# Performance work log

Measured on AMD Instinct MI355X. Metric: run time of the kernel, lower is better.

## Reference

```python
import jax, jax.numpy as jnp
import numpy as np

STRIDE = 4
HEADS = 8
KSIZE = 5
PAD_L = 4  # causal: kernel_size - 1


def _layernorm(x, g, b, eps=1e-5):
    mu = jnp.mean(x, axis=-1, keepdims=True)
    var = jnp.mean((x - mu) ** 2, axis=-1, keepdims=True)
    return (x - mu) * jax.lax.rsqrt(var + eps) * g + b


def setup_inputs() -> dict:
    key = jax.random.key(0)
    ks = jax.random.split(key, 6)
    B, T, C = 8, 2048, 1024
    D = 4096
    x = jax.random.normal(ks[0], (B, T, C), dtype=jnp.float32)
    W_proj = jax.random.normal(ks[1], (C * STRIDE, D), dtype=jnp.float32) * 0.02
    b_proj = jnp.zeros((D,), dtype=jnp.float32)
    ln_g = jnp.ones((D,), dtype=jnp.float32)
    ln_b = jnp.zeros((D,), dtype=jnp.float32)
    W_wgen = jax.random.normal(ks[2], (D, HEADS * KSIZE), dtype=jnp.float32) * 0.02
    b_wgen = jnp.zeros((HEADS * KSIZE,), dtype=jnp.float32)
    W_ff = jax.random.normal(ks[3], (D, D), dtype=jnp.float32) * 0.02
    b_ff = jnp.zeros((D,), dtype=jnp.float32)
    return {"x": x, "W_proj": W_proj, "b_proj": b_proj, "ln_g": ln_g, "ln_b": ln_b,
            "W_wgen": W_wgen, "b_wgen": b_wgen, "W_ff": W_ff, "b_ff": b_ff}


def reference(x, W_proj, b_proj, ln_g, ln_b, W_wgen, b_wgen, W_ff, b_ff):
    B, T, C = x.shape
    folded_T = T // STRIDE
    # fold time into channels, then dense projection to llm_dim
    xf = x[:, : folded_T * STRIDE].reshape(B, folded_T, C * STRIDE)
    h = xf @ W_proj + b_proj  # [B, Tf, D]
    D = h.shape[-1]
    R = D // HEADS
    # LConv1DBlock with norm_before + dynamic conv + (linear, relu, dropout p=0) + residual
    res = h
    y = _layernorm(h, ln_g, ln_b)
    # per-position dynamic weights, softmax over kernel taps
    w = (y @ W_wgen + b_wgen).reshape(B, folded_T, HEADS, KSIZE)
    w = jax.nn.softmax(w, axis=-1)  # [B, Tf, H, K]
    # causal depthwise conv: out[t] = sum_k w[t,k] * y[t - (K-1) + k]
    yp = jnp.pad(y, ((0, 0), (PAD_L, 0), (0, 0)))  # left pad time
    # stacked taps: [K, B, Tf, H, R]
    taps = jnp.stack([yp[:, k:k + folded_T] for k in range(KSIZE)], axis=0)
    taps = taps.reshape(KSIZE, B, folded_T, HEADS, R)
    conv = jnp.einsum('kbthr,bthk->bthr', taps, w).reshape(B, folded_T, D)
    # feed-forward ops: linear -> relu -> dropout(p=0)
    out = res + jax.nn.relu(conv @ W_ff + b_ff)
    return out
```

## Files before the change

kernel.cpp:

```cpp
#include <hip/hip_runtime.h>

typedef unsigned short u16;
typedef unsigned int u32;
typedef __attribute__((ext_vector_type(8))) short bf16x8;
typedef __attribute__((ext_vector_type(4))) float f32x4;

__device__ __forceinline__ float bf2f(u16 u) {
    union { u32 i; float f; } x; x.i = ((u32)u) << 16; return x.f;
}
__device__ __forceinline__ u16 f2bf(float f) {
    union { float f; u32 i; } x; x.f = f;
    u32 u = x.i;
    u += 0x7FFFu + ((u >> 16) & 1u);
    return (u16)(u >> 16);
}
__device__ __forceinline__ float wred(float v) {
    #pragma unroll
    for (int off = 32; off; off >>= 1) v += __shfl_down(v, off);
    return v;
}
__device__ __forceinline__ void gload_lds16(const void* g, void* l) {
    __builtin_amdgcn_global_load_lds(
        (const __attribute__((address_space(1))) u32*)g,
        (__attribute__((address_space(3))) u32*)l,
        16, 0, 0);
}

__global__ __launch_bounds__(256)
void prep(const float* __restrict__ x, u16* __restrict__ xb,
          const float* __restrict__ Wp, u16* __restrict__ WpT,
          const float* __restrict__ Wf, u16* __restrict__ WfT,
          const float* __restrict__ Wg, float* __restrict__ WgT) {
    __shared__ float tile[64][65];
    int b = blockIdx.x;
    int tid = threadIdx.x;
    if (b < 16384) {
        int i = (b * 256 + tid) * 4;
        float4 v = *(const float4*)(x + i);
        ushort4 p;
        p.x = f2bf(v.x); p.y = f2bf(v.y); p.z = f2bf(v.z); p.w = f2bf(v.w);
        *(ushort4*)(xb + i) = p;
    } else if (b < 24576) {
        const float* W = (b < 20480) ? Wp : Wf;
        u16* Wt = (b < 20480) ? WpT : WfT;
        int bid = (b < 20480) ? (b - 16384) : (b - 20480);
        int n0 = (bid & 63) * 64;
        int k0 = (bid >> 6) * 64;
        int tx = tid & 31, ty = tid >> 5;
        #pragma unroll
        for (int i = 0; i < 8; ++i) {
            int kk = ty + i * 8;
            const float* src = W + (size_t)(k0 + kk) * 4096 + n0;
            tile[kk][tx]      = src[tx];
            tile[kk][tx + 32] = src[tx + 32];
        }
        __syncthreads();
        #pragma unroll
        for (int i = 0; i < 8; ++i) {
            int nn = ty + i * 8;
            ushort2 p;
            p.x = f2bf(tile[tx * 2][nn]);
            p.y = f2bf(tile[tx * 2 + 1][nn]);
            *(ushort2*)(Wt + (size_t)(n0 + nn) * 4096 + k0 + tx * 2) = p;
        }
    } else {
        int idx = (b - 24576) * 256 + tid;
        int c = idx >> 12, e = idx & 4095;
        WgT[idx] = Wg[(size_t)e * 40 + c];
    }
}

template <int MODE>
__global__ __launch_bounds__(512, 2)
void gemm256(const u16* __restrict__ A, const u16* __restrict__ Bt,
             const float* __restrict__ bias, const void* __restrict__ res,
             void* __restrict__ outv) {
    const int K = 4096, N = 4096;
    __shared__ u16 smem[65536];

    const int tid = threadIdx.x;
    const int lane = tid & 63;
    const int w = tid >> 6;
    const int wr = w >> 2, wc = w & 3;
    const int fr = lane & 15;
    const int fk = (lane >> 4) * 8;
    const int cswz = (fr & 7) << 3;

    const int bid = blockIdx.x;
    const int swz = (bid & 7) * (gridDim.x >> 3) + (bid >> 3);
    const int tm = swz >> 4, tn = swz & 15;
    const size_t rowA0 = (size_t)tm * 256;
    const size_t rowB0 = (size_t)tn * 256;

    const int srl = lane >> 3;
    const int scl = ((lane & 7) ^ srl) << 3;

    f32x4 acc[8][4] = {};
    bf16x8 af[8];
    bf16x8 bh0[4];
    bf16x8 bh1[4];

    auto stA = [&](int b, int half, int kt) {
        #pragma unroll
        for (int i = 0; i < 2; ++i) {
            size_t grow = rowA0 + half * 128 + i * 64 + w * 8 + srl;
            gload_lds16(A + grow * K + kt * 64 + scl,
                        &smem[b * 32768 + half * 8192 + i * 4096 + w * 512 + lane * 8]);
        }
    };
    auto stB = [&](int b, int half, int kt) {
        #pragma unroll
        for (int i = 0; i < 2; ++i) {
            size_t grow = rowB0 + half * 128 + i * 64 + w * 8 + srl;
            gload_lds16(Bt + grow * K + kt * 64 + scl,
                        &smem[b * 32768 + 16384 + half * 8192 + i * 4096 + w * 512 + lane * 8]);
        }
    };
    auto ldA = [&](int b, int qm) {
        #pragma unroll
        for (int kk = 0; kk < 2; ++kk)
            #pragma unroll
            for (int m = 0; m < 4; ++m) {
                int base = b * 32768 + (wr * 128 + (qm * 4 + m) * 16 + fr) * 64;
                af[m * 2 + kk] = *(const bf16x8*)&smem[base + ((kk * 32 + fk) ^ cswz)];
            }
    };
    auto ldB = [&](int b, int qn, bf16x8 (&bh)[4]) {
        #pragma unroll
        for (int kk = 0; kk < 2; ++kk)
            #pragma unroll
            for (int n = 0; n < 2; ++n) {
                int base = b * 32768 + 16384 + (wc * 64 + qn * 32 + n * 16 + fr) * 64;
                bh[n * 2 + kk] = *(const bf16x8*)&smem[base + ((kk * 32 + fk) ^ cswz)];
            }
    };
    auto ldAB = [&](int b, int qm, int qn, bf16x8 (&bh)[4]) {
        #pragma unroll
        for (int kk = 0; kk < 2; ++kk) {
            #pragma unroll
            for (int m = 0; m < 4; ++m) {
                int base = b * 32768 + (wr * 128 + (qm * 4 + m) * 16 + fr) * 64;
                af[m * 2 + kk] = *(const bf16x8*)&smem[base + ((kk * 32 + fk) ^ cswz)];
            }
            #pragma unroll
            for (int n = 0; n < 2; ++n) {
                int base = b * 32768 + 16384 + (wc * 64 + qn * 32 + n * 16 + fr) * 64;
                bh[n * 2 + kk] = *(const bf16x8*)&smem[base + ((kk * 32 + fk) ^ cswz)];
            }
        }
    };
    auto mma = [&](int qm, int qn, bf16x8 (&bh)[4]) {
        __builtin_amdgcn_s_setprio(1);
        #pragma unroll
        for (int kk = 0; kk < 2; ++kk)
            #pragma unroll
            for (int m = 0; m < 4; ++m)
                #pragma unroll
                for (int n = 0; n < 2; ++n)
                    acc[qm*4+m][qn*2+n] = __builtin_amdgcn_mfma_f32_16x16x32_bf16(
                        af[m*2+kk], bh[n*2+kk], acc[qm*4+m][qn*2+n], 0, 0, 0);
        __builtin_amdgcn_s_setprio(0);
    };
    #define BAR() __builtin_amdgcn_s_barrier()
    #define VM4() asm volatile("s_waitcnt vmcnt(4)" ::: "memory")

    stB(0, 0, 0); stB(0, 1, 0); stA(0, 0, 0); stA(0, 1, 0);
    stB(1, 0, 1); stB(1, 1, 1);
    VM4();
    BAR();

    for (int i = 0; i < 32; ++i) {
        const int t = 2 * i;
        const int kt2 = (t + 2 < 64) ? t + 2 : 63;
        const int kt3 = (t + 3 < 64) ? t + 3 : 63;
        ldAB(0, 0, 0, bh0);
        stA(1, 0, t + 1);
        BAR(); mma(0, 0, bh0);
        ldB(0, 1, bh1);
        stA(1, 1, t + 1);
        BAR(); mma(0, 1, bh1);
        ldA(0, 1);
        stB(0, 0, kt2);
        BAR(); mma(1, 1, bh1);
        stB(0, 1, kt2);
        VM4();
        BAR(); mma(1, 0, bh0);
        ldAB(1, 0, 0, bh0);
        stA(0, 0, kt2);
        BAR(); mma(0, 0, bh0);
        ldB(1, 1, bh1);
        stA(0, 1, kt2);
        BAR(); mma(0, 1, bh1);
        ldA(1, 1);
        stB(1, 0, kt3);
        BAR(); mma(1, 1, bh1);
        stB(1, 1, kt3);
        VM4();
        BAR(); mma(1, 0, bh0);
    }
    #undef BAR
    #undef VM4

    const int cc = lane & 15;
    const int cr = (lane >> 4) * 4;
    #pragma unroll
    for (int m = 0; m < 8; ++m) {
        #pragma unroll
        for (int n = 0; n < 4; ++n) {
            size_t row = rowA0 + wr * 128 + m * 16 + cr;
            size_t col = rowB0 + wc * 64 + n * 16 + cc;
            float bv = bias[col];
            #pragma unroll
            for (int q = 0; q < 4; ++q) {
                size_t idx = (row + q) * (size_t)N + col;
                float v = acc[m][n][q] + bv;
                if (MODE == 1) v = ((const float*)res)[idx] + fmaxf(v, 0.0f);
                if (MODE == 3) v = bf2f(((const u16*)res)[idx]) + fmaxf(v, 0.0f);
                if (MODE == 2) ((u16*)outv)[idx] = f2bf(v);
                else           ((float*)outv)[idx] = v;
            }
        }
    }
}

template <bool HB>
__global__ __launch_bounds__(256)
void ln_wgen(const void* __restrict__ hv, const float* __restrict__ g,
             const float* __restrict__ beta, const float* __restrict__ WgT,
             const float* __restrict__ bg, u16* __restrict__ y,
             float* __restrict__ w) {
    __shared__ u32 ylp[8][2048];
    __shared__ float red[8];
    __shared__ float wraw[8][40];

    int tid = threadIdx.x, lane = tid & 63, wv = tid >> 6;
    size_t row0 = (size_t)blockIdx.x * 8;

    for (int r = 0; r < 8; ++r) {
        float vals[16];
        float s = 0.f, ss = 0.f;
        if (HB) {
            const u16* hr = (const u16*)hv + (row0 + r) * 4096;
            #pragma unroll
            for (int i = 0; i < 2; ++i) {
                uint4 u = *(const uint4*)(hr + (size_t)(tid + i * 256) * 8);
                const u16* us = (const u16*)&u;
                #pragma unroll
                for (int j = 0; j < 8; ++j) {
                    float f = bf2f(us[j]);
                    vals[i * 8 + j] = f;
                    s += f; ss += f * f;
                }
            }
        } else {
            const float4* hr = (const float4*)((const float*)hv + (row0 + r) * 4096);
            #pragma unroll
            for (int i = 0; i < 4; ++i) {
                float4 v = hr[tid + i * 256];
                vals[i*4+0] = v.x; vals[i*4+1] = v.y; vals[i*4+2] = v.z; vals[i*4+3] = v.w;
                s  += v.x + v.y + v.z + v.w;
                ss += v.x*v.x + v.y*v.y + v.z*v.z + v.w*v.w;
            }
        }
        s = wred(s); ss = wred(ss);
        if (lane == 0) { red[wv] = s; red[4 + wv] = ss; }
        __syncthreads();
        float S = red[0] + red[1] + red[2] + red[3];
        float SS = red[4] + red[5] + red[6] + red[7];
        float mu = S * (1.0f / 4096.0f);
        float var = SS * (1.0f / 4096.0f) - mu * mu;
        float inv = rsqrtf(var + 1e-5f);
        u16* yr = y + (row0 + r) * 4096;
        if (HB) {
            #pragma unroll
            for (int i = 0; i < 2; ++i) {
                int e0 = i * 2048 + tid * 8;
                u32 words[4];
                #pragma unroll
                for (int k = 0; k < 4; ++k) {
                    float2 gv = *(const float2*)(g + e0 + k * 2);
                    float2 bv = *(const float2*)(beta + e0 + k * 2);
                    float o0 = (vals[i*8 + k*2]     - mu) * inv * gv.x + bv.x;
                    float o1 = (vals[i*8 + k*2 + 1] - mu) * inv * gv.y + bv.y;
                    words[k] = (u32)f2bf(o0) | ((u32)f2bf(o1) << 16);
                    ylp[r][e0 / 2 + k] = words[k];
                }
                uint4 pk; pk.x = words[0]; pk.y = words[1]; pk.z = words[2]; pk.w = words[3];
                *(uint4*)(yr + e0) = pk;
            }
        } else {
            #pragma unroll
            for (int i = 0; i < 4; ++i) {
                int base = tid + i * 256;
                float4 gv = ((const float4*)g)[base];
                float4 bv = ((const float4*)beta)[base];
                float o0 = (vals[i*4+0] - mu) * inv * gv.x + bv.x;
                float o1 = (vals[i*4+1] - mu) * inv * gv.y + bv.y;
                float o2 = (vals[i*4+2] - mu) * inv * gv.z + bv.z;
                float o3 = (vals[i*4+3] - mu) * inv * gv.w + bv.w;
                u32 p01 = (u32)f2bf(o0) | ((u32)f2bf(o1) << 16);
                u32 p23 = (u32)f2bf(o2) | ((u32)f2bf(o3) << 16);
                ylp[r][base * 2]     = p01;
                ylp[r][base * 2 + 1] = p23;
                uint2 pk; pk.x = p01; pk.y = p23;
                *(uint2*)(yr + base * 4) = pk;
            }
        }
        __syncthreads();
    }

    float acc[8][10];
    #pragma unroll
    for (int r = 0; r < 8; ++r)
        #pragma unroll
        for (int c = 0; c < 10; ++c) acc[r][c] = 0.f;

    for (int eb = lane; eb < 2048; eb += 64) {
        float alo[8], ahi[8];
        #pragma unroll
        for (int r = 0; r < 8; ++r) {
            u32 a = ylp[r][eb];
            alo[r] = bf2f((u16)a);
            ahi[r] = bf2f((u16)(a >> 16));
        }
        #pragma unroll
        for (int c0 = 0; c0 < 10; ++c0) {
            int c = wv * 10 + c0;
            float2 wg = ((const float2*)(WgT + (size_t)c * 4096))[eb];
            #pragma unroll
            for (int r = 0; r < 8; ++r)
                acc[r][c0] += alo[r] * wg.x + ahi[r] * wg.y;
        }
    }
    #pragma unroll
    for (int r = 0; r < 8; ++r) {
        #pragma unroll
        for (int c0 = 0; c0 < 10; ++c0) {
            float p = wred(acc[r][c0]);
            if (lane == 0) wraw[r][wv * 10 + c0] = p + bg[wv * 10 + c0];
        }
    }
    __syncthreads();

    if (tid < 64) {
        int r = tid >> 3, hh = tid & 7;
        float e5[5];
        float mx = -1e30f;
        #pragma unroll
        for (int k = 0; k < 5; ++k) mx = fmaxf(mx, wraw[r][hh * 5 + k]);
        float sum = 0.f;
        #pragma unroll
        for (int k = 0; k < 5; ++k) { e5[k] = expf(wraw[r][hh * 5 + k] - mx); sum += e5[k]; }
        float isum = 1.0f / sum;
        float* wp = w + (row0 + r) * 40 + hh * 5;
        #pragma unroll
        for (int k = 0; k < 5; ++k) wp[k] = e5[k] * isum;
    }
}

__global__ __launch_bounds__(256)
void dconv3(const u16* __restrict__ y, const float* __restrict__ w,
            u16* __restrict__ conv) {
    int bid = blockIdx.x;
    int half = bid & 1;
    int rem = bid >> 1;
    int tc = rem & 31, b = rem >> 5;
    int t0 = tc * 16;
    int d0 = half * 2048 + threadIdx.x * 8;
    int head = d0 >> 9;
    const u16* yb = y + (size_t)b * 512 * 4096 + d0;
    u16* cb = conv + (size_t)b * 512 * 4096 + d0;
    const float* wb = w + ((size_t)b * 512) * 40 + head * 5;

    float r0[8], r1[8], r2[8], r3[8], r4[8];
    {
        float* slots[4] = { r1, r2, r3, r4 };
        #pragma unroll
        for (int j = 0; j < 4; ++j) {
            int tt = t0 - 4 + j;
            if (tt >= 0) {
                uint4 v = *(const uint4*)(yb + (size_t)tt * 4096);
                const u16* us = (const u16*)&v;
                #pragma unroll
                for (int e = 0; e < 8; ++e) slots[j][e] = bf2f(us[e]);
            } else {
                #pragma unroll
                for (int e = 0; e < 8; ++e) slots[j][e] = 0.f;
            }
        }
    }

    #pragma unroll
    for (int tt = 0; tt < 16; ++tt) {
        int t = t0 + tt;
        #pragma unroll
        for (int e = 0; e < 8; ++e) {
            r0[e] = r1[e]; r1[e] = r2[e]; r2[e] = r3[e]; r3[e] = r4[e];
        }
        uint4 v = *(const uint4*)(yb + (size_t)t * 4096);
        const u16* us = (const u16*)&v;
        #pragma unroll
        for (int e = 0; e < 8; ++e) r4[e] = bf2f(us[e]);
        const float* wt = wb + (size_t)t * 40;
        float w0 = wt[0], w1 = wt[1], w2 = wt[2], w3 = wt[3], w4 = wt[4];
        u16 o[8];
        #pragma unroll
        for (int e = 0; e < 8; ++e) {
            float a = w0 * r0[e] + w1 * r1[e] + w2 * r2[e] + w3 * r3[e] + w4 * r4[e];
            o[e] = f2bf(a);
        }
        *(uint4*)(cb + (size_t)t * 4096) = *(uint4*)o;
    }
}

extern "C" void kernel_launch(void* const* d_in, const int* in_sizes, int n_in,
                              void* d_out, int out_size, void* d_ws, size_t ws_size,
                              hipStream_t stream) {
    const float* x      = (const float*)d_in[0];
    const float* W_proj = (const float*)d_in[1];
    const float* b_proj = (const float*)d_in[2];
    const float* ln_g   = (const float*)d_in[3];
    const float* ln_b   = (const float*)d_in[4];
    const float* W_wgen = (const float*)d_in[5];
    const float* b_wgen = (const float*)d_in[6];
    const float* W_ff   = (const float*)d_in[7];
    const float* b_ff   = (const float*)d_in[8];
    float* out = (float*)d_out;

    char* ws = (char*)d_ws;
    u16* xb   = (u16*)(ws);
    u16* WpT  = (u16*)(ws + ((size_t)32 << 20));
    u16* WfT  = (u16*)(ws + ((size_t)64 << 20));
    float* wbuf = (float*)(ws + ((size_t)96 << 20));
    float* WgT  = (float*)(ws + ((size_t)97 << 20));
    u16* hb   = (u16*)(ws + ((size_t)98 << 20));
    u16* conv = xb;
    u16* ybuf = WpT;

    prep<<<25216, 256, 0, stream>>>(x, xb, W_proj, WpT, W_ff, WfT, W_wgen, WgT);

    if (ws_size >= ((size_t)131 << 20)) {
        gemm256<2><<<256, 512, 0, stream>>>(xb, WpT, b_proj, nullptr, hb);
        ln_wgen<true><<<512, 256, 0, stream>>>(hb, ln_g, ln_b, WgT, b_wgen, ybuf, wbuf);
        dconv3<<<512, 256, 0, stream>>>(ybuf, wbuf, conv);
        gemm256<3><<<256, 512, 0, stream>>>(conv, WfT, b_ff, hb, out);
    } else {
        gemm256<0><<<256, 512, 0, stream>>>(xb, WpT, b_proj, nullptr, out);
        ln_wgen<false><<<512, 256, 0, stream>>>(out, ln_g, ln_b, WgT, b_wgen, ybuf, wbuf);
        dconv3<<<512, 256, 0, stream>>>(ybuf, wbuf, conv);
        gemm256<1><<<256, 512, 0, stream>>>(conv, WfT, b_ff, out, out);
    }
}
```

Baseline: 338.6 us.

## Fuse depthwise conv into layernorm kernel and stage bf16 GEMM epilogue through LDS

The dynamic convolution is merged into the layernorm/weight-generation kernel. Each block keeps its 8 normalized rows in LDS and recomputes the layernorm of the 4 preceding rows from h as a halo, so the y and softmax-weight buffers are no longer written to and re-read from global memory, and one launch is removed. The cost is redundant halo loads and reductions per block. Separately, the bf16-output GEMM epilogue now writes through swizzled shared memory so global stores are coalesced 16-byte rows instead of scattered 2-byte stores.

```diff
diff --git a/kernel.cpp b/kernel.cpp
--- a/kernel.cpp
+++ b/kernel.cpp
@@ -203,21 +203,48 @@
 
     const int cc = lane & 15;
     const int cr = (lane >> 4) * 4;
-    #pragma unroll
-    for (int m = 0; m < 8; ++m) {
-        #pragma unroll
-        for (int n = 0; n < 4; ++n) {
-            size_t row = rowA0 + wr * 128 + m * 16 + cr;
-            size_t col = rowB0 + wc * 64 + n * 16 + cc;
-            float bv = bias[col];
-            #pragma unroll
-            for (int q = 0; q < 4; ++q) {
-                size_t idx = (row + q) * (size_t)N + col;
-                float v = acc[m][n][q] + bv;
-                if (MODE == 1) v = ((const float*)res)[idx] + fmaxf(v, 0.0f);
-                if (MODE == 3) v = bf2f(((const u16*)res)[idx]) + fmaxf(v, 0.0f);
-                if (MODE == 2) ((u16*)outv)[idx] = f2bf(v);
-                else           ((float*)outv)[idx] = v;
+    if (MODE == 2) {
+        __builtin_amdgcn_s_barrier();
+        #pragma unroll
+        for (int m = 0; m < 8; ++m) {
+            #pragma unroll
+            for (int n = 0; n < 4; ++n) {
+                int lc = wc * 64 + n * 16 + cc;
+                float bv = bias[rowB0 + lc];
+                #pragma unroll
+                for (int q = 0; q < 4; ++q) {
+                    int lr = wr * 128 + m * 16 + cr + q;
+                    int sc = (lc & 7) | (((lc >> 3) ^ (lr & 7)) << 3);
+                    smem[lr * 256 + sc] = f2bf(acc[m][n][q] + bv);
+                }
+            }
+        }
+        __builtin_amdgcn_s_barrier();
+        u16* ob = (u16*)outv;
+        #pragma unroll
+        for (int it = 0; it < 16; ++it) {
+            int idx = it * 512 + tid;
+            int lr = idx >> 5;
+            int c16 = idx & 31;
+            uint4 v = *(uint4*)&smem[lr * 256 + ((c16 ^ (lr & 7)) * 8)];
+            *(uint4*)(ob + (rowA0 + lr) * (size_t)N + rowB0 + c16 * 8) = v;
+        }
+    } else {
+        #pragma unroll
+        for (int m = 0; m < 8; ++m) {
+            #pragma unroll
+            for (int n = 0; n < 4; ++n) {
+                size_t row = rowA0 + wr * 128 + m * 16 + cr;
+                size_t col = rowB0 + wc * 64 + n * 16 + cc;
+                float bv = bias[col];
+                #pragma unroll
+                for (int q = 0; q < 4; ++q) {
+                    size_t idx = (row + q) * (size_t)N + col;
+                    float v = acc[m][n][q] + bv;
+                    if (MODE == 1) v = ((const float*)res)[idx] + fmaxf(v, 0.0f);
+                    if (MODE == 3) v = bf2f(((const u16*)res)[idx]) + fmaxf(v, 0.0f);
+                    ((float*)outv)[idx] = v;
+                }
             }
         }
     }
@@ -225,16 +252,18 @@
 
 template <bool HB>
 __global__ __launch_bounds__(256)
-void ln_wgen(const void* __restrict__ hv, const float* __restrict__ g,
+void ln_conv(const void* __restrict__ hv, const float* __restrict__ g,
              const float* __restrict__ beta, const float* __restrict__ WgT,
-             const float* __restrict__ bg, u16* __restrict__ y,
-             float* __restrict__ w) {
+             const float* __restrict__ bg, u16* __restrict__ conv) {
     __shared__ u32 ylp[8][2048];
     __shared__ float red[8];
     __shared__ float wraw[8][40];
+    __shared__ float wsm[8][40];
+    __shared__ float pmv[4][2];
 
     int tid = threadIdx.x, lane = tid & 63, wv = tid >> 6;
     size_t row0 = (size_t)blockIdx.x * 8;
+    int t0 = (int)(row0 & 511);
 
     for (int r = 0; r < 8; ++r) {
         float vals[16];
@@ -270,23 +299,18 @@
         float mu = S * (1.0f / 4096.0f);
         float var = SS * (1.0f / 4096.0f) - mu * mu;
         float inv = rsqrtf(var + 1e-5f);
-        u16* yr = y + (row0 + r) * 4096;
         if (HB) {
             #pragma unroll
             for (int i = 0; i < 2; ++i) {
                 int e0 = i * 2048 + tid * 8;
-                u32 words[4];
                 #pragma unroll
                 for (int k = 0; k < 4; ++k) {
                     float2 gv = *(const float2*)(g + e0 + k * 2);
                     float2 bv = *(const float2*)(beta + e0 + k * 2);
                     float o0 = (vals[i*8 + k*2]     - mu) * inv * gv.x + bv.x;
                     float o1 = (vals[i*8 + k*2 + 1] - mu) * inv * gv.y + bv.y;
-                    words[k] = (u32)f2bf(o0) | ((u32)f2bf(o1) << 16);
-                    ylp[r][e0 / 2 + k] = words[k];
-                }
-                uint4 pk; pk.x = words[0]; pk.y = words[1]; pk.z = words[2]; pk.w = words[3];
-                *(uint4*)(yr + e0) = pk;
+                    ylp[r][e0 / 2 + k] = (u32)f2bf(o0) | ((u32)f2bf(o1) << 16);
+                }
             }
         } else {
             #pragma unroll
@@ -298,15 +322,48 @@
                 float o1 = (vals[i*4+1] - mu) * inv * gv.y + bv.y;
                 float o2 = (vals[i*4+2] - mu) * inv * gv.z + bv.z;
                 float o3 = (vals[i*4+3] - mu) * inv * gv.w + bv.w;
-                u32 p01 = (u32)f2bf(o0) | ((u32)f2bf(o1) << 16);
-                u32 p23 = (u32)f2bf(o2) | ((u32)f2bf(o3) << 16);
-                ylp[r][base * 2]     = p01;
-                ylp[r][base * 2 + 1] = p23;
-                uint2 pk; pk.x = p01; pk.y = p23;
-                *(uint2*)(yr + base * 4) = pk;
+                ylp[r][base * 2]     = (u32)f2bf(o0) | ((u32)f2bf(o1) << 16);
+                ylp[r][base * 2 + 1] = (u32)f2bf(o2) | ((u32)f2bf(o3) << 16);
             }
         }
         __syncthreads();
+    }
+
+    if (t0 > 0) {
+        for (int r = 0; r < 4; ++r) {
+            size_t row = row0 - 4 + r;
+            float s = 0.f, ss = 0.f;
+            if (HB) {
+                const u16* hr = (const u16*)hv + row * 4096;
+                #pragma unroll
+                for (int i = 0; i < 2; ++i) {
+                    uint4 u = *(const uint4*)(hr + (size_t)(tid + i * 256) * 8);
+                    const u16* us = (const u16*)&u;
+                    #pragma unroll
+                    for (int j = 0; j < 8; ++j) { float f = bf2f(us[j]); s += f; ss += f * f; }
+                }
+            } else {
+                const float4* hr = (const float4*)((const float*)hv + row * 4096);
+                #pragma unroll
+                for (int i = 0; i < 4; ++i) {
+                    float4 v = hr[tid + i * 256];
+                    s  += v.x + v.y + v.z + v.w;
+                    ss += v.x*v.x + v.y*v.y + v.z*v.z + v.w*v.w;
+                }
+            }
+            s = wred(s); ss = wred(ss);
+            if (lane == 0) { red[wv] = s; red[4 + wv] = ss; }
+            __syncthreads();
+            if (tid == 0) {
+                float S = red[0] + red[1] + red[2] + red[3];
+                float SS = red[4] + red[5] + red[6] + red[7];
+                float mu = S * (1.0f / 4096.0f);
+                float var = SS * (1.0f / 4096.0f) - mu * mu;
+                pmv[r][0] = mu;
+                pmv[r][1] = rsqrtf(var + 1e-5f);
+            }
+            __syncthreads();
+        }
     }
 
     float acc[8][10];
@@ -352,64 +409,67 @@
         #pragma unroll
         for (int k = 0; k < 5; ++k) { e5[k] = expf(wraw[r][hh * 5 + k] - mx); sum += e5[k]; }
         float isum = 1.0f / sum;
-        float* wp = w + (row0 + r) * 40 + hh * 5;
-        #pragma unroll
-        for (int k = 0; k < 5; ++k) wp[k] = e5[k] * isum;
-    }
-}
-
-__global__ __launch_bounds__(256)
-void dconv3(const u16* __restrict__ y, const float* __restrict__ w,
-            u16* __restrict__ conv) {
-    int bid = blockIdx.x;
-    int half = bid & 1;
-    int rem = bid >> 1;
-    int tc = rem & 31, b = rem >> 5;
-    int t0 = tc * 16;
-    int d0 = half * 2048 + threadIdx.x * 8;
-    int head = d0 >> 9;
-    const u16* yb = y + (size_t)b * 512 * 4096 + d0;
-    u16* cb = conv + (size_t)b * 512 * 4096 + d0;
-    const float* wb = w + ((size_t)b * 512) * 40 + head * 5;
-
-    float r0[8], r1[8], r2[8], r3[8], r4[8];
-    {
-        float* slots[4] = { r1, r2, r3, r4 };
-        #pragma unroll
-        for (int j = 0; j < 4; ++j) {
-            int tt = t0 - 4 + j;
-            if (tt >= 0) {
-                uint4 v = *(const uint4*)(yb + (size_t)tt * 4096);
-                const u16* us = (const u16*)&v;
-                #pragma unroll
-                for (int e = 0; e < 8; ++e) slots[j][e] = bf2f(us[e]);
-            } else {
-                #pragma unroll
-                for (int e = 0; e < 8; ++e) slots[j][e] = 0.f;
-            }
-        }
-    }
-
-    #pragma unroll
-    for (int tt = 0; tt < 16; ++tt) {
-        int t = t0 + tt;
-        #pragma unroll
-        for (int e = 0; e < 8; ++e) {
-            r0[e] = r1[e]; r1[e] = r2[e]; r2[e] = r3[e]; r3[e] = r4[e];
-        }
-        uint4 v = *(const uint4*)(yb + (size_t)t * 4096);
-        const u16* us = (const u16*)&v;
-        #pragma unroll
-        for (int e = 0; e < 8; ++e) r4[e] = bf2f(us[e]);
-        const float* wt = wb + (size_t)t * 40;
-        float w0 = wt[0], w1 = wt[1], w2 = wt[2], w3 = wt[3], w4 = wt[4];
-        u16 o[8];
-        #pragma unroll
-        for (int e = 0; e < 8; ++e) {
-            float a = w0 * r0[e] + w1 * r1[e] + w2 * r2[e] + w3 * r3[e] + w4 * r4[e];
-            o[e] = f2bf(a);
-        }
-        *(uint4*)(cb + (size_t)t * 4096) = *(uint4*)o;
+        #pragma unroll
+        for (int k = 0; k < 5; ++k) wsm[r][hh * 5 + k] = e5[k] * isum;
+    }
+    __syncthreads();
+
+    for (int half = 0; half < 2; ++half) {
+        int d0 = half * 2048 + tid * 8;
+        int head = d0 >> 9;
+        float yp[4][8];
+        #pragma unroll
+        for (int r = 0; r < 4; ++r)
+            #pragma unroll
+            for (int e = 0; e < 8; ++e) yp[r][e] = 0.f;
+        if (t0 > 0) {
+            float gv[8], bv[8];
+            #pragma unroll
+            for (int k = 0; k < 2; ++k) {
+                float4 gq = *(const float4*)(g + d0 + k * 4);
+                float4 bq = *(const float4*)(beta + d0 + k * 4);
+                gv[k*4+0]=gq.x; gv[k*4+1]=gq.y; gv[k*4+2]=gq.z; gv[k*4+3]=gq.w;
+                bv[k*4+0]=bq.x; bv[k*4+1]=bq.y; bv[k*4+2]=bq.z; bv[k*4+3]=bq.w;
+            }
+            #pragma unroll
+            for (int r = 0; r < 4; ++r) {
+                float mu = pmv[r][0], inv = pmv[r][1];
+                if (HB) {
+                    uint4 u = *(const uint4*)((const u16*)hv + (row0 - 4 + r) * 4096 + d0);
+                    const u16* us = (const u16*)&u;
+                    #pragma unroll
+                    for (int e = 0; e < 8; ++e)
+                        yp[r][e] = bf2f(f2bf((bf2f(us[e]) - mu) * inv * gv[e] + bv[e]));
+                } else {
+                    const float* hr = (const float*)hv + (row0 - 4 + r) * 4096 + d0;
+                    #pragma unroll
+                    for (int e = 0; e < 8; ++e)
+                        yp[r][e] = bf2f(f2bf((hr[e] - mu) * inv * gv[e] + bv[e]));
+                }
+            }
+        }
+        #pragma unroll
+        for (int ri = 0; ri < 8; ++ri) {
+            float a[8] = {0.f,0.f,0.f,0.f,0.f,0.f,0.f,0.f};
+            #pragma unroll
+            for (int k = 0; k < 5; ++k) {
+                int src = ri - 4 + k;
+                float w_ = wsm[ri][head * 5 + k];
+                if (src >= 0) {
+                    uint4 u = *(const uint4*)&ylp[src][d0 >> 1];
+                    const u16* us = (const u16*)&u;
+                    #pragma unroll
+                    for (int e = 0; e < 8; ++e) a[e] += w_ * bf2f(us[e]);
+                } else {
+                    #pragma unroll
+                    for (int e = 0; e < 8; ++e) a[e] += w_ * yp[src + 4][e];
+                }
+            }
+            u16 o[8];
+            #pragma unroll
+            for (int e = 0; e < 8; ++e) o[e] = f2bf(a[e]);
+            *(uint4*)(conv + (row0 + ri) * 4096 + d0) = *(uint4*)o;
+        }
     }
 }
 
@@ -431,23 +491,19 @@
     u16* xb   = (u16*)(ws);
     u16* WpT  = (u16*)(ws + ((size_t)32 << 20));
     u16* WfT  = (u16*)(ws + ((size_t)64 << 20));
-    float* wbuf = (float*)(ws + ((size_t)96 << 20));
-    float* WgT  = (float*)(ws + ((size_t)97 << 20));
-    u16* hb   = (u16*)(ws + ((size_t)98 << 20));
+    float* WgT  = (float*)(ws + ((size_t)96 << 20));
+    u16* hb   = (u16*)(ws + ((size_t)97 << 20));
     u16* conv = xb;
-    u16* ybuf = WpT;
 
     prep<<<25216, 256, 0, stream>>>(x, xb, W_proj, WpT, W_ff, WfT, W_wgen, WgT);
 
-    if (ws_size >= ((size_t)131 << 20)) {
+    if (ws_size >= ((size_t)129 << 20)) {
         gemm256<2><<<256, 512, 0, stream>>>(xb, WpT, b_proj, nullptr, hb);
-        ln_wgen<true><<<512, 256, 0, stream>>>(hb, ln_g, ln_b, WgT, b_wgen, ybuf, wbuf);
-        dconv3<<<512, 256, 0, stream>>>(ybuf, wbuf, conv);
+        ln_conv<true><<<512, 256, 0, stream>>>(hb, ln_g, ln_b, WgT, b_wgen, conv);
         gemm256<3><<<256, 512, 0, stream>>>(conv, WfT, b_ff, hb, out);
     } else {
         gemm256<0><<<256, 512, 0, stream>>>(xb, WpT, b_proj, nullptr, out);
-        ln_wgen<false><<<512, 256, 0, stream>>>(out, ln_g, ln_b, WgT, b_wgen, ybuf, wbuf);
-        dconv3<<<512, 256, 0, stream>>>(ybuf, wbuf, conv);
+        ln_conv<false><<<512, 256, 0, stream>>>(out, ln_g, ln_b, WgT, b_wgen, conv);
         gemm256<1><<<256, 512, 0, stream>>>(conv, WfT, b_ff, out, out);
     }
 }
```

Measured after the change: 334.5 us. Within noise of the previous version (-1.2%).
